# Optimization experiments

Measured on AMD Instinct MI355X. Metric: run time of the kernel, lower is better.

## Reference

```python
import jax, jax.numpy as jnp
import numpy as np

EMBED = 256
HEADS = 8
LAYERS = 6
FFN = 1024
LEVELS = 4
POINTS = 4
SHAPES = [(128, 128), (64, 64), (32, 32), (16, 16)]


def setup_inputs() -> dict:
    key = jax.random.key(0)
    ks = jax.random.split(key, 32)
    B = 2
    inp = {}
    for i, (h, w) in enumerate(SHAPES):
        inp[f'src{i}'] = jax.random.normal(ks[i], (B, EMBED, h, w), jnp.float32)
        inp[f'pos{i}'] = jax.random.normal(ks[4 + i], (B, EMBED, h, w), jnp.float32)
    s = 0.02
    inp['level_embed'] = jax.random.normal(ks[8], (LEVELS, EMBED), jnp.float32) * s
    inp['Wv'] = jax.random.normal(ks[9], (LAYERS, EMBED, EMBED), jnp.float32) * s
    inp['bv'] = jnp.zeros((LAYERS, EMBED), jnp.float32)
    inp['Woff'] = jax.random.normal(ks[10], (LAYERS, EMBED, HEADS * LEVELS * POINTS * 2), jnp.float32) * s
    inp['boff'] = jax.random.normal(ks[11], (LAYERS, HEADS * LEVELS * POINTS * 2), jnp.float32) * 0.5
    inp['Waw'] = jax.random.normal(ks[12], (LAYERS, EMBED, HEADS * LEVELS * POINTS), jnp.float32) * s
    inp['baw'] = jnp.zeros((LAYERS, HEADS * LEVELS * POINTS), jnp.float32)
    inp['Wout'] = jax.random.normal(ks[13], (LAYERS, EMBED, EMBED), jnp.float32) * s
    inp['bout'] = jnp.zeros((LAYERS, EMBED), jnp.float32)
    inp['gamma'] = jnp.ones((LAYERS, EMBED), jnp.float32)
    inp['beta'] = jnp.zeros((LAYERS, EMBED), jnp.float32)
    inp['W1'] = jax.random.normal(ks[14], (LAYERS, EMBED, FFN), jnp.float32) * s
    inp['b1'] = jnp.zeros((LAYERS, FFN), jnp.float32)
    inp['W2'] = jax.random.normal(ks[15], (LAYERS, FFN, EMBED), jnp.float32) * s
    inp['b2'] = jnp.zeros((LAYERS, EMBED), jnp.float32)
    return inp


def _layernorm(x, g, b, eps=1e-5):
    mu = x.mean(-1, keepdims=True)
    var = ((x - mu) ** 2).mean(-1, keepdims=True)
    return (x - mu) * jax.lax.rsqrt(var + eps) * g + b


def _bilinear_sample(value, loc, Hl, Wl):
    # value: [B, heads, S_l, Dh]; loc: [B, Len, heads, P, 2] normalized to [0,1]
    # grid_sample semantics: align_corners=False, zero padding
    B, Len, heads, P, _ = loc.shape
    Dh = value.shape[-1]
    x = loc[..., 0] * Wl - 0.5
    y = loc[..., 1] * Hl - 0.5
    x0 = jnp.floor(x)
    y0 = jnp.floor(y)
    dx = x - x0
    dy = y - y0
    x0i = x0.astype(jnp.int32)
    y0i = y0.astype(jnp.int32)
    out = jnp.zeros((B, heads, Len, P, Dh), value.dtype)
    corners = [(x0i, y0i, (1 - dx) * (1 - dy)), (x0i + 1, y0i, dx * (1 - dy)),
               (x0i, y0i + 1, (1 - dx) * dy), (x0i + 1, y0i + 1, dx * dy)]
    for xi, yi, w in corners:
        valid = (xi >= 0) & (xi < Wl) & (yi >= 0) & (yi < Hl)
        idx = jnp.clip(yi, 0, Hl - 1) * Wl + jnp.clip(xi, 0, Wl - 1)  # [B,Len,heads,P]
        idx_t = idx.transpose(0, 2, 1, 3).reshape(B, heads, Len * P)
        g = jnp.take_along_axis(value, idx_t[..., None], axis=2)  # [B,heads,Len*P,Dh]
        g = g.reshape(B, heads, Len, P, Dh)
        wv = jnp.where(valid, w, 0.0).transpose(0, 2, 1, 3)[..., None]  # [B,heads,Len,P,1]
        out = out + g * wv
    return out


def reference(src0, src1, src2, src3, pos0, pos1, pos2, pos3, level_embed,
              Wv, bv, Woff, boff, Waw, baw, Wout, bout, gamma, beta, W1, b1, W2, b2):
    srcs = [src0, src1, src2, src3]
    poss = [pos0, pos1, pos2, pos3]
    B, C = src0.shape[0], src0.shape[1]
    shapes = [(s.shape[2], s.shape[3]) for s in srcs]
    L = len(shapes)
    heads, P = HEADS, POINTS
    Dh = C // heads
    x = jnp.concatenate([s.reshape(B, C, -1).transpose(0, 2, 1) for s in srcs], axis=1)  # [B,Len,C]
    pos_flat = jnp.concatenate(
        [p.reshape(B, C, -1).transpose(0, 2, 1) + level_embed[l][None, None, :]
         for l, p in enumerate(poss)], axis=1)
    starts = np.concatenate([[0], np.cumsum([h * w for h, w in shapes])[:-1]]).tolist()
    # reference points (valid_ratios are all ones since masks are all-False)
    refs = []
    for (H, W) in shapes:
        yy, xx = jnp.meshgrid(jnp.linspace(0.5, H - 0.5, H), jnp.linspace(0.5, W - 0.5, W), indexing='ij')
        refs.append(jnp.stack([xx.reshape(-1) / W, yy.reshape(-1) / H], axis=-1))
    ref = jnp.concatenate(refs, axis=0)  # [Len,2]
    normalizer = jnp.array([[w, h] for h, w in shapes], dtype=x.dtype)  # [L,2]
    Len = x.shape[1]
    for li in range(LAYERS):
        q = x + pos_flat
        off = (q @ Woff[li] + boff[li]).reshape(B, Len, heads, L, P, 2)
        aw = jax.nn.softmax((q @ Waw[li] + baw[li]).reshape(B, Len, heads, L * P), axis=-1)
        aw = aw.reshape(B, Len, heads, L, P)
        loc = ref[None, :, None, None, None, :] + off / normalizer[None, None, None, :, None, :]
        v = (x @ Wv[li] + bv[li]).reshape(B, Len, heads, Dh).transpose(0, 2, 1, 3)  # [B,heads,Len,Dh]
        acc = jnp.zeros((B, heads, Len, Dh), x.dtype)
        for lvl, (H, W) in enumerate(shapes):
            s0 = starts[lvl]
            vl = v[:, :, s0:s0 + H * W, :]
            samp = _bilinear_sample(vl, loc[:, :, :, lvl], H, W)  # [B,heads,Len,P,Dh]
            awl = aw[:, :, :, lvl].transpose(0, 2, 1, 3)  # [B,heads,Len,P]
            acc = acc + (samp * awl[..., None]).sum(axis=3)
        attn_out = acc.transpose(0, 2, 1, 3).reshape(B, Len, C) @ Wout[li] + bout[li]
        x = x + attn_out  # dropout is identity at eval
        x = _layernorm(x, gamma[li], beta[li])
        x = jax.nn.relu(x @ W1[li] + b1[li]) @ W2[li] + b2[li]  # Mlp output (no residual, per source)
    return x
```

## Files before the change

kernel.cpp:

```cpp
#include <hip/hip_runtime.h>

#define LEN 21760
#define MROWS 43520
#define WSTRIDE 753664

typedef __attribute__((ext_vector_type(8))) short s8v;
typedef __attribute__((ext_vector_type(4))) short s4v;
typedef __attribute__((ext_vector_type(4))) float f4v;
typedef __attribute__((ext_vector_type(4))) unsigned u4v;

__device__ inline float bf2f(short u){
  union { unsigned u; float f; } v; v.u = ((unsigned)(unsigned short)u) << 16; return v.f;
}
__device__ inline short f2bf(float f){
  union { float f; unsigned u; } v; v.f = f;
  unsigned r = v.u + 0x7fffu + ((v.u >> 16) & 1u);
  return (short)(r >> 16);
}
__device__ inline void gload_lds16(const short* g, short* l){
  __builtin_amdgcn_global_load_lds((const __attribute__((address_space(1))) void*)g,
                                   (__attribute__((address_space(3))) void*)l, 16, 0, 0);
}

__global__ __launch_bounds__(256) void prep_kernel(
    const float* __restrict__ s0,const float* __restrict__ s1,
    const float* __restrict__ s2,const float* __restrict__ s3,
    const float* __restrict__ p0,const float* __restrict__ p1,
    const float* __restrict__ p2,const float* __restrict__ p3,
    const float* __restrict__ le,
    short* __restrict__ xbf, short* __restrict__ posb,
    short* __restrict__ q)
{
  __shared__ float xs[64][65];
  __shared__ float ps[64][65];
  const int n0 = blockIdx.x * 64;
  const int b  = blockIdx.y;
  const int t  = threadIdx.x;

  int l, s0n, lw;
  if (n0 < 16384){ l=0; s0n=0; lw=7; }
  else if (n0 < 20480){ l=1; s0n=16384; lw=6; }
  else if (n0 < 21504){ l=2; s0n=20480; lw=5; }
  else { l=3; s0n=21504; lw=4; }
  const int pbase = n0 - s0n;
  const long HW = 1L << (2*lw);
  const float* sp = (l==0?s0:(l==1?s1:(l==2?s2:s3)));
  const float* pp = (l==0?p0:(l==1?p1:(l==2?p2:p3)));

  for (int ch0 = 0; ch0 < 256; ch0 += 64){
    __syncthreads();
    #pragma unroll
    for (int cc = 0; cc < 4; cc++){
      int cl = cc*16 + (t >> 4);
      int quad = t & 15;
      int ch = ch0 + cl;
      long gi = (long)(b*256 + ch)*HW + pbase + quad*4;
      f4v xv = *(const f4v*)&sp[gi];
      f4v pv = *(const f4v*)&pp[gi];
      float lec = le[l*256 + ch];
      *(f4v*)&xs[cl][quad*4] = xv;
      f4v pe; pe[0]=pv[0]+lec; pe[1]=pv[1]+lec; pe[2]=pv[2]+lec; pe[3]=pv[3]+lec;
      *(f4v*)&ps[cl][quad*4] = pe;
    }
    __syncthreads();
    #pragma unroll
    for (int cc = 0; cc < 4; cc++){
      int pi = t >> 2;
      int cl = cc*16 + (t & 3)*4;
      long row = (long)b*LEN + n0 + pi;
      int col = ch0 + cl;
      s4v xv, pv, qv;
      #pragma unroll
      for (int j=0;j<4;j++){
        float xf = xs[cl+j][pi];
        float pf = ps[cl+j][pi];
        xv[j] = f2bf(xf); pv[j] = f2bf(pf);
        qv[j] = f2bf(xf + pf);
      }
      *(s4v*)&xbf[row*256 + col]  = xv;
      *(s4v*)&posb[row*256 + col] = pv;
      *(s4v*)&q[row*256 + col]    = qv;
    }
  }
}

__global__ __launch_bounds__(256) void convw_kernel(
    const float* __restrict__ Woff, const float* __restrict__ Waw,
    const float* __restrict__ Wv, const float* __restrict__ Wout,
    const float* __restrict__ W1, const float* __restrict__ W2,
    const float* __restrict__ boff, const float* __restrict__ baw,
    short* __restrict__ wts, float* __restrict__ biasOA)
{
  const int id = blockIdx.x;
  if (id >= 1104){
    int li = id - 1104;
    for (int i = threadIdx.x; i < 384; i += 256)
      biasOA[li*384 + i] = (i < 256) ? boff[li*256 + i] : baw[li*128 + (i-256)];
    return;
  }
  __shared__ float ls[64][65];
  const int li = id / 184;
  int r = id % 184;
  const float* src; short* dst; int N, K;
  if (r < 16)      {          src=Woff+li*65536;  dst=wts+(size_t)li*WSTRIDE;        N=256;  K=256;  }
  else if (r < 24) { r-=16;   src=Waw +li*32768;  dst=wts+(size_t)li*WSTRIDE+65536;  N=128;  K=256;  }
  else if (r < 40) { r-=24;   src=Wv  +li*65536;  dst=wts+(size_t)li*WSTRIDE+98304;  N=256;  K=256;  }
  else if (r < 56) { r-=40;   src=Wout+li*65536;  dst=wts+(size_t)li*WSTRIDE+163840; N=256;  K=256;  }
  else if (r < 120){ r-=56;   src=W1  +li*262144; dst=wts+(size_t)li*WSTRIDE+229376; N=1024; K=256;  }
  else             { r-=120;  src=W2  +li*262144; dst=wts+(size_t)li*WSTRIDE+491520; N=256;  K=1024; }
  const int ntn = N >> 6;
  const int tn = r % ntn, tk = r / ntn;
  const int n0 = tn*64, k0 = tk*64;
  const int t = threadIdx.x;
  const int rr = t >> 4;
  const int c4 = (t & 15) * 4;
  #pragma unroll
  for (int it = 0; it < 4; it++){
    int row = it*16 + rr;
    f4v v = *(const f4v*)&src[(long)(k0+row)*N + n0 + c4];
    ls[row][c4] = v[0]; ls[row][c4+1] = v[1]; ls[row][c4+2] = v[2]; ls[row][c4+3] = v[3];
  }
  __syncthreads();
  #pragma unroll
  for (int it = 0; it < 4; it++){
    int nrow = it*16 + rr;
    s4v o;
    #pragma unroll
    for (int j=0;j<4;j++) o[j] = f2bf(ls[c4+j][nrow]);
    *(s4v*)&dst[(long)(n0+nrow)*K + k0 + c4] = o;
  }
}

template<bool RELU, bool OUT_BF16, bool EMIT_Q>
__global__ __launch_bounds__(256) void gemm_bf16(
    const short* __restrict__ A, const short* __restrict__ Wt,
    const float* __restrict__ bias,
    void* __restrict__ Cout, const short* __restrict__ posb,
    short* __restrict__ qout,
    int M, int N, int K, int NT)
{
  __shared__ short As[128*64];
  __shared__ short Bs[128*64];
  const int p = blockIdx.x, nwg = gridDim.x;
  const int xq = nwg >> 3, xr = nwg & 7;
  const int xx = p & 7, xs2 = p >> 3;
  const int l = ((xx < xr) ? xx*(xq+1) : xr*(xq+1) + (xx-xr)*xq) + xs2;
  const int m0 = (l / NT) * 128;
  const int n0 = (l % NT) * 128;

  const int t = threadIdx.x;
  const int lane = t & 63, wv = t >> 6;
  const int wm = (wv >> 1) * 64, wn = (wv & 1) * 64;
  const int fr = lane & 15, fg = lane >> 4;
  const int srow = lane >> 3;
  const int schunk = (lane & 7) ^ (srow & 7);

  f4v acc[4][4];
  #pragma unroll
  for (int i=0;i<4;i++)
    #pragma unroll
    for (int j=0;j<4;j++) acc[i][j] = (f4v){0.f,0.f,0.f,0.f};

  for (int k0 = 0; k0 < K; k0 += 64) {
    __syncthreads();
    #pragma unroll
    for (int i=0;i<4;i++){
      int seg = wv*4 + i;
      int row = seg*8 + srow;
      gload_lds16(&A [(long)(m0+row)*K + k0 + schunk*8], &As[seg*512]);
      gload_lds16(&Wt[(long)(n0+row)*K + k0 + schunk*8], &Bs[seg*512]);
    }
    __syncthreads();
    #pragma unroll
    for (int kk=0; kk<64; kk+=32){
      s8v ar[4], br[4];
      #pragma unroll
      for (int i=0;i<4;i++){
        int r = wm + i*16 + fr;
        int ch = ((kk>>3) + fg) ^ (fr & 7);
        ar[i] = *(const s8v*)&As[r*64 + ch*8];
      }
      #pragma unroll
      for (int j=0;j<4;j++){
        int r = wn + j*16 + fr;
        int ch = ((kk>>3) + fg) ^ (fr & 7);
        br[j] = *(const s8v*)&Bs[r*64 + ch*8];
      }
      #pragma unroll
      for (int i=0;i<4;i++)
        #pragma unroll
        for (int j=0;j<4;j++)
          acc[i][j] = __builtin_amdgcn_mfma_f32_16x16x32_bf16(ar[i], br[j], acc[i][j], 0,0,0);
    }
  }
  #pragma unroll
  for (int i=0;i<4;i++){
    #pragma unroll
    for (int j=0;j<4;j++){
      int col = n0 + wn + j*16 + fr;
      float bcol = bias[col];
      #pragma unroll
      for (int r=0;r<4;r++){
        long row = m0 + wm + i*16 + fg*4 + r;
        float vv = acc[i][j][r] + bcol;
        if (RELU) vv = fmaxf(vv, 0.f);
        if (OUT_BF16) ((short*)Cout)[row*N + col] = f2bf(vv);
        else ((float*)Cout)[row*N + col] = vv;
        if (EMIT_Q){
          qout[row*N + col] = f2bf(vv + bf2f(posb[row*N + col]));
        }
      }
    }
  }
}

__global__ __launch_bounds__(512) void gemm_out_ln(
    const short* __restrict__ A, const short* __restrict__ Wt,
    const float* __restrict__ bias, const short* __restrict__ resid,
    const float* __restrict__ gamma, const float* __restrict__ beta,
    short* __restrict__ xln)
{
  const int K = 256;
  __shared__ short As[128*64];
  __shared__ short Bs[256*64];
  const int m0 = blockIdx.x * 128;
  const int t = threadIdx.x;
  const int lane = t & 63, wv = t >> 6;
  const int wm = wv * 16;
  const int fr = lane & 15, fg = lane >> 4;
  const int srow = lane >> 3;
  const int schunk = (lane & 7) ^ (srow & 7);

  f4v acc[16];
  #pragma unroll
  for (int j=0;j<16;j++) acc[j] = (f4v){0.f,0.f,0.f,0.f};

  for (int k0 = 0; k0 < K; k0 += 64) {
    __syncthreads();
    #pragma unroll
    for (int i=0;i<2;i++){
      int seg = wv*2 + i;
      int row = seg*8 + srow;
      gload_lds16(&A[(long)(m0+row)*K + k0 + schunk*8], &As[seg*512]);
    }
    #pragma unroll
    for (int i=0;i<4;i++){
      int seg = wv*4 + i;
      int row = seg*8 + srow;
      gload_lds16(&Wt[(long)row*K + k0 + schunk*8], &Bs[seg*512]);
    }
    __syncthreads();
    #pragma unroll
    for (int kk=0; kk<64; kk+=32){
      int ch = ((kk>>3) + fg);
      s8v ar = *(const s8v*)&As[(wm + fr)*64 + ((ch ^ (fr & 7)))*8];
      #pragma unroll
      for (int j=0;j<16;j++){
        s8v br = *(const s8v*)&Bs[(j*16 + fr)*64 + ((ch ^ (fr & 7)))*8];
        acc[j] = __builtin_amdgcn_mfma_f32_16x16x32_bf16(ar, br, acc[j], 0,0,0);
      }
    }
  }
  #pragma unroll
  for (int r=0;r<4;r++){
    long row = m0 + wm + fg*4 + r;
    float vals[16];
    float s = 0.f;
    #pragma unroll
    for (int j=0;j<16;j++){
      int col = j*16 + fr;
      float vv = acc[j][r] + bias[col] + bf2f(resid[row*256 + col]);
      vals[j] = vv; s += vv;
    }
    #pragma unroll
    for (int o=1;o<16;o<<=1) s += __shfl_xor(s, o, 64);
    float mu = s * (1.f/256.f);
    float s2 = 0.f;
    #pragma unroll
    for (int j=0;j<16;j++){ float d = vals[j]-mu; vals[j] = d; s2 += d*d; }
    #pragma unroll
    for (int o=1;o<16;o<<=1) s2 += __shfl_xor(s2, o, 64);
    float rstd = rsqrtf(s2*(1.f/256.f) + 1e-5f);
    #pragma unroll
    for (int j=0;j<16;j++){
      int col = j*16 + fr;
      xln[row*256 + col] = f2bf(vals[j]*rstd*gamma[col] + beta[col]);
    }
  }
}

__global__ __launch_bounds__(256) void sample_kernel(const short* __restrict__ v,
                const short* __restrict__ offaw, short* __restrict__ accO)
{
  const int t = threadIdx.x;
  const int qi = t >> 5;
  const int tq = t & 31;
  const int head = tq >> 2, cg = tq & 3;
  const int bid = blockIdx.x;
  const int n = ((bid & 7) * 340 + (bid >> 3)) * 8 + qi;
  const int b = blockIdx.y;
  const long m = (long)b*LEN + n;
  const short* oa = offaw + m*384;

  s8v or0 = *(const s8v*)&oa[head*32];
  s8v or1 = *(const s8v*)&oa[head*32 + 8];
  s8v or2 = *(const s8v*)&oa[head*32 + 16];
  s8v or3 = *(const s8v*)&oa[head*32 + 24];
  float off_f[32];
  #pragma unroll
  for (int i=0;i<8;i++){
    off_f[i]    = bf2f(or0[i]);
    off_f[8+i]  = bf2f(or1[i]);
    off_f[16+i] = bf2f(or2[i]);
    off_f[24+i] = bf2f(or3[i]);
  }

  s8v lg0 = *(const s8v*)&oa[256 + head*16];
  s8v lg1 = *(const s8v*)&oa[256 + head*16 + 8];
  float logit[16];
  #pragma unroll
  for (int i=0;i<8;i++){ logit[i] = bf2f(lg0[i]); logit[8+i] = bf2f(lg1[i]); }
  float mx = -1e30f;
  #pragma unroll
  for (int j=0;j<16;j++) mx = fmaxf(mx, logit[j]);
  float ssum = 0.f;
  #pragma unroll
  for (int j=0;j<16;j++){ logit[j] = __expf(logit[j]-mx); ssum += logit[j]; }
  float inv = 1.f/ssum;

  int s0n, lwn;
  if (n < 16384){ s0n=0; lwn=7; }
  else if (n < 20480){ s0n=16384; lwn=6; }
  else if (n < 21504){ s0n=20480; lwn=5; }
  else { s0n=21504; lwn=4; }
  int p = n - s0n;
  int Wn = 1 << lwn;
  float refx = ((p & (Wn-1)) + 0.5f) / Wn;
  float refy = ((p >> lwn) + 0.5f) / Wn;

  const int starts[4] = {0,16384,20480,21504};
  float acc[8];
  #pragma unroll
  for (int c=0;c<8;c++) acc[c] = 0.f;

  #pragma unroll
  for (int l=0;l<4;l++){
    const int W = 128 >> l, Wm1 = W - 1;
    const short* vb = v + ((long)b*LEN + starts[l])*256 + head*32 + cg*8;
    #pragma unroll
    for (int pp=0;pp<4;pp++){
      int j = l*4 + pp;
      float sx = refx * W + off_f[j*2]     - 0.5f;
      float sy = refy * W + off_f[j*2 + 1] - 0.5f;
      float fx0 = floorf(sx), fy0 = floorf(sy);
      float dx = sx - fx0, dy = sy - fy0;
      int x0 = (int)fx0, y0 = (int)fy0;
      int x0c = min(max(x0,0),Wm1),   x1c = min(max(x0+1,0),Wm1);
      int y0c = min(max(y0,0),Wm1),   y1c = min(max(y0+1,0),Wm1);
      float aw = logit[j] * inv;
      float r0w = ((unsigned)y0     < (unsigned)W) ? (1.f-dy)*aw : 0.f;
      float r1w = ((unsigned)(y0+1) < (unsigned)W) ? dy*aw       : 0.f;
      float c0w = ((unsigned)x0     < (unsigned)W) ? (1.f-dx)    : 0.f;
      float c1w = ((unsigned)(x0+1) < (unsigned)W) ? dx          : 0.f;
      float w00 = r0w*c0w, w10 = r0w*c1w, w01 = r1w*c0w, w11 = r1w*c1w;
      const short* r0p = vb + (long)(y0c*W)*256;
      const short* r1p = vb + (long)(y1c*W)*256;
      u4v g00 = *(const u4v*)&r0p[x0c*256];
      u4v g10 = *(const u4v*)&r0p[x1c*256];
      u4v g01 = *(const u4v*)&r1p[x0c*256];
      u4v g11 = *(const u4v*)&r1p[x1c*256];
      #pragma unroll
      for (int c=0;c<4;c++){
        union {unsigned u; float f;} lo00,hi00,lo10,hi10,lo01,hi01,lo11,hi11;
        lo00.u = g00[c] << 16;  hi00.u = g00[c];
        lo10.u = g10[c] << 16;  hi10.u = g10[c];
        lo01.u = g01[c] << 16;  hi01.u = g01[c];
        lo11.u = g11[c] << 16;  hi11.u = g11[c];
        acc[2*c]   += w00*lo00.f + w10*lo10.f + w01*lo01.f + w11*lo11.f;
        acc[2*c+1] += w00*hi00.f + w10*hi10.f + w01*hi01.f + w11*hi11.f;
      }
    }
  }
  s8v o;
  #pragma unroll
  for (int c=0;c<8;c++) o[c] = f2bf(acc[c]);
  *(s8v*)&accO[m*256 + head*32 + cg*8] = o;
}

extern "C" void kernel_launch(void* const* d_in, const int* in_sizes, int n_in,
                              void* d_out, int out_size, void* d_ws, size_t ws_size,
                              hipStream_t stream)
{
  const float* s0   = (const float*)d_in[0];
  const float* p0   = (const float*)d_in[1];
  const float* s1   = (const float*)d_in[2];
  const float* p1   = (const float*)d_in[3];
  const float* s2   = (const float*)d_in[4];
  const float* p2   = (const float*)d_in[5];
  const float* s3   = (const float*)d_in[6];
  const float* p3   = (const float*)d_in[7];
  const float* le   = (const float*)d_in[8];
  const float* Wv   = (const float*)d_in[9];
  const float* bv   = (const float*)d_in[10];
  const float* Woff = (const float*)d_in[11];
  const float* boff = (const float*)d_in[12];
  const float* Waw  = (const float*)d_in[13];
  const float* baw  = (const float*)d_in[14];
  const float* Wout = (const float*)d_in[15];
  const float* bout = (const float*)d_in[16];
  const float* gamma= (const float*)d_in[17];
  const float* beta = (const float*)d_in[18];
  const float* W1   = (const float*)d_in[19];
  const float* b1   = (const float*)d_in[20];
  const float* W2   = (const float*)d_in[21];
  const float* b2   = (const float*)d_in[22];

  char* wsb = (char*)d_ws;
  short* xbf   = (short*)(wsb);
  short* posb  = (short*)(wsb + 22282240);
  short* qxln  = (short*)(wsb + 44564480);
  short* vbf   = (short*)(wsb + 66846720);
  short* accb  = (short*)(wsb + 89128960);
  short* offawh= (short*)(wsb + 111411200);
  short* hbuf  = (short*)(wsb + 66846720);
  short* wts   = (short*)(wsb + 155975680);
  float* biasOA= (float*)(wsb + 165019648);

  prep_kernel<<<dim3(340,2),256,0,stream>>>(s0,s1,s2,s3,p0,p1,p2,p3,le,xbf,posb,qxln);
  convw_kernel<<<1110,256,0,stream>>>(Woff,Waw,Wv,Wout,W1,W2,boff,baw,wts,biasOA);

  for (int li = 0; li < 6; li++){
    const short* wl = wts + (size_t)li*WSTRIDE;
    gemm_bf16<false,true,false><<<1020,256,0,stream>>>(
        qxln, wl, biasOA+li*384, offawh, nullptr,nullptr, MROWS, 384, 256, 3);
    gemm_bf16<false,true,false><<<680,256,0,stream>>>(
        xbf, wl+98304, bv+li*256, vbf, nullptr,nullptr, MROWS, 256, 256, 2);
    sample_kernel<<<dim3(LEN/8,2),256,0,stream>>>(vbf, offawh, accb);
    gemm_out_ln<<<340,512,0,stream>>>(accb, wl+163840, bout+li*256, xbf,
                                      gamma+li*256, beta+li*256, qxln);
    gemm_bf16<true,true,false><<<2720,256,0,stream>>>(
        qxln, wl+229376, b1+li*1024, hbuf, nullptr,nullptr, MROWS, 1024, 256, 8);
    if (li < 5){
      gemm_bf16<false,true,true><<<680,256,0,stream>>>(
          hbuf, wl+491520, b2+li*256, xbf, posb, qxln, MROWS, 256, 1024, 2);
    } else {
      gemm_bf16<false,false,false><<<680,256,0,stream>>>(
          hbuf, wl+491520, b2+li*256, (float*)d_out, nullptr,nullptr, MROWS, 256, 1024, 2);
    }
  }
}
```

Baseline: 1.414 ms.

## Fuse FFN up and down projections into one kernel with LDS-resident hidden

Replaces the two FFN GEMM launches with a single kernel. Each block of 128 rows loads its layer-normed input into LDS, computes the 1024-wide ReLU hidden in four 256-wide chunks, and accumulates the W2 projection directly. This removes the global-memory round trip of the large hidden activation buffer and one launch per layer. In exchange it uses about 144KB of LDS per block, which limits occupancy to one block per CU. It also has only 340 blocks, serialized weight loads with frequent barriers, and no double buffering.

```diff
diff --git a/kernel.cpp b/kernel.cpp
--- a/kernel.cpp
+++ b/kernel.cpp
@@ -285,6 +285,113 @@
     for (int j=0;j<16;j++){
       int col = j*16 + fr;
       xln[row*256 + col] = f2bf(vals[j]*rstd*gamma[col] + beta[col]);
+    }
+  }
+}
+
+template<bool LAST>
+__global__ __launch_bounds__(512) void fused_ffn(
+    const short* __restrict__ xln, const short* __restrict__ W1g,
+    const short* __restrict__ W2g,
+    const float* __restrict__ b1, const float* __restrict__ b2,
+    const short* __restrict__ posb,
+    short* __restrict__ xbf, short* __restrict__ qout,
+    float* __restrict__ outf)
+{
+  __shared__ short Als[128*256];
+  __shared__ short Hls[128*256];
+  __shared__ short Wls[256*32];
+  const int m0 = blockIdx.x * 128;
+  const int t = threadIdx.x;
+  const int lane = t & 63, wv = t >> 6;
+  const int wm = wv * 16;
+  const int fr = lane & 15, fg = lane >> 4;
+
+  {
+    int srow = t >> 5;
+    int c = t & 31;
+    #pragma unroll
+    for (int it = 0; it < 8; it++){
+      int rrow = it*16 + srow;
+      int csrc = c ^ (rrow & 7);
+      gload_lds16(&xln[(long)(m0+rrow)*256 + csrc*8], &Als[it*4096 + t*8]);
+    }
+  }
+
+  f4v oacc[16];
+  #pragma unroll
+  for (int j=0;j<16;j++) oacc[j] = (f4v){0.f,0.f,0.f,0.f};
+
+  const int wrow = t >> 2;
+  const int wc = t & 3;
+
+  for (int hc = 0; hc < 4; hc++){
+    f4v hacc[16];
+    #pragma unroll
+    for (int j=0;j<16;j++) hacc[j] = (f4v){0.f,0.f,0.f,0.f};
+    for (int k0 = 0; k0 < 256; k0 += 32){
+      __syncthreads();
+      #pragma unroll
+      for (int it = 0; it < 2; it++){
+        int rrow = it*128 + wrow;
+        int csrc = wc ^ (rrow & 3);
+        gload_lds16(&W1g[(long)(hc*256 + rrow)*256 + k0 + csrc*8], &Wls[it*4096 + t*8]);
+      }
+      __syncthreads();
+      int arow = wm + fr;
+      s8v ar = *(const s8v*)&Als[arow*256 + ((((k0>>3)+fg) ^ (arow&7)))*8];
+      #pragma unroll
+      for (int j=0;j<16;j++){
+        int brow = j*16 + fr;
+        s8v br = *(const s8v*)&Wls[brow*32 + ((fg ^ (brow&3)))*8];
+        hacc[j] = __builtin_amdgcn_mfma_f32_16x16x32_bf16(ar, br, hacc[j], 0,0,0);
+      }
+    }
+    #pragma unroll
+    for (int j=0;j<16;j++){
+      int col = j*16 + fr;
+      float bb = b1[hc*256 + col];
+      #pragma unroll
+      for (int r=0;r<4;r++){
+        int row = wm + fg*4 + r;
+        float vv = fmaxf(hacc[j][r] + bb, 0.f);
+        int ch = (col >> 3) ^ (row & 7);
+        Hls[row*256 + ch*8 + (col & 7)] = f2bf(vv);
+      }
+    }
+    for (int k0 = 0; k0 < 256; k0 += 32){
+      __syncthreads();
+      #pragma unroll
+      for (int it = 0; it < 2; it++){
+        int rrow = it*128 + wrow;
+        int csrc = wc ^ (rrow & 3);
+        gload_lds16(&W2g[(long)rrow*1024 + hc*256 + k0 + csrc*8], &Wls[it*4096 + t*8]);
+      }
+      __syncthreads();
+      int arow = wm + fr;
+      s8v ar = *(const s8v*)&Hls[arow*256 + ((((k0>>3)+fg) ^ (arow&7)))*8];
+      #pragma unroll
+      for (int j=0;j<16;j++){
+        int brow = j*16 + fr;
+        s8v br = *(const s8v*)&Wls[brow*32 + ((fg ^ (brow&3)))*8];
+        oacc[j] = __builtin_amdgcn_mfma_f32_16x16x32_bf16(ar, br, oacc[j], 0,0,0);
+      }
+    }
+  }
+  #pragma unroll
+  for (int j=0;j<16;j++){
+    int col = j*16 + fr;
+    float bb = b2[col];
+    #pragma unroll
+    for (int r=0;r<4;r++){
+      long row = m0 + wm + fg*4 + r;
+      float vv = oacc[j][r] + bb;
+      if (LAST){
+        outf[row*256 + col] = vv;
+      } else {
+        xbf[row*256 + col]  = f2bf(vv);
+        qout[row*256 + col] = f2bf(vv + bf2f(posb[row*256 + col]));
+      }
     }
   }
 }
@@ -422,7 +529,6 @@
   short* vbf   = (short*)(wsb + 66846720);
   short* accb  = (short*)(wsb + 89128960);
   short* offawh= (short*)(wsb + 111411200);
-  short* hbuf  = (short*)(wsb + 66846720);
   short* wts   = (short*)(wsb + 155975680);
   float* biasOA= (float*)(wsb + 165019648);
 
@@ -438,14 +544,14 @@
     sample_kernel<<<dim3(LEN/8,2),256,0,stream>>>(vbf, offawh, accb);
     gemm_out_ln<<<340,512,0,stream>>>(accb, wl+163840, bout+li*256, xbf,
                                       gamma+li*256, beta+li*256, qxln);
-    gemm_bf16<true,true,false><<<2720,256,0,stream>>>(
-        qxln, wl+229376, b1+li*1024, hbuf, nullptr,nullptr, MROWS, 1024, 256, 8);
     if (li < 5){
-      gemm_bf16<false,true,true><<<680,256,0,stream>>>(
-          hbuf, wl+491520, b2+li*256, xbf, posb, qxln, MROWS, 256, 1024, 2);
+      fused_ffn<false><<<340,512,0,stream>>>(
+          qxln, wl+229376, wl+491520, b1+li*1024, b2+li*256,
+          posb, xbf, qxln, nullptr);
     } else {
-      gemm_bf16<false,false,false><<<680,256,0,stream>>>(
-          hbuf, wl+491520, b2+li*256, (float*)d_out, nullptr,nullptr, MROWS, 256, 1024, 2);
-    }
-  }
-}
+      fused_ffn<true><<<340,512,0,stream>>>(
+          qxln, wl+229376, wl+491520, b1+li*1024, b2+li*256,
+          nullptr, nullptr, nullptr, (float*)d_out);
+    }
+  }
+}
```

After: 1.750 ms. +23.7%, slower.
